# Performance work log

Measured on AMD Instinct MI355X. Metric: run time of the kernel, lower is better.

The kernel has to match this reference:

```python
import jax, jax.numpy as jnp
import numpy as np
from jax import lax

NEG_INF = -10000.0  # matches the torch code's fill value


def setup_inputs() -> dict:
    key = jax.random.key(0)
    k1, k2, k3 = jax.random.split(key, 3)
    B, T, L = 512, 512, 102  # n_labels = vocab_size(100) + 2
    logits = jax.random.normal(k1, (B, T, L), dtype=jnp.float32)
    transitions = jax.random.normal(k2, (L, L), dtype=jnp.float32)
    lens = jax.random.randint(k3, (B,), 0, 512, dtype=jnp.int32)
    return {"logits": logits, "transitions": transitions, "lens": lens}


def reference(logits, transitions, lens):
    """Linear-chain CRF partition function (forward algorithm).

    logits: [B, T, L] emission scores (L = n_labels incl. start/stop)
    transitions: [L, L], transitions[j, k] = score of k -> j
    lens: [B] int sequence lengths
    returns: [B] log partition function
    """
    B, T, L = logits.shape
    start_idx, stop_idx = L - 2, L - 1

    alpha0 = jnp.full((B, L), NEG_INF, dtype=logits.dtype).at[:, start_idx].set(0.0)

    def step(carry, logit_t):
        alpha, c_lens = carry  # alpha: [B, L], logit_t: [B, L]
        # mat[b, j, k] = transitions[j, k] + alpha[b, k]
        mat = transitions[None, :, :] + alpha[:, None, :]
        alpha_nxt = logit_t + jax.scipy.special.logsumexp(mat, axis=2)  # [B, L]
        alive = (c_lens > 0)[:, None]
        alpha = jnp.where(alive, alpha_nxt, alpha)
        return (alpha, c_lens - 1), None

    (alpha, _), _ = lax.scan(step, (alpha0, lens), jnp.swapaxes(logits, 0, 1))

    alpha = alpha + transitions[stop_idx][None, :]
    norm = jax.scipy.special.logsumexp(alpha, axis=1)  # [B]
    return norm
```

## Files before the change

kernel.cpp:

```cpp
#include <hip/hip_runtime.h>


typedef float f32x2 __attribute__((ext_vector_type(2)));
typedef float f32x4 __attribute__((ext_vector_type(4)));

#define CRF_L 102
#define CRF_RP 104
#define CRF_START 100
#define CRF_STOP 101
#define NEG_BIG (-1.0e30f)
#define LN2F 0.6931471805599453f

#define REP25(X) X(0) X(1) X(2) X(3) X(4) X(5) X(6) X(7) X(8) X(9) X(10) \
                 X(11) X(12) X(13) X(14) X(15) X(16) X(17) X(18) X(19) \
                 X(20) X(21) X(22) X(23) X(24)

template <int CTRL>
__device__ __forceinline__ float dpp_add_step(float x) {
    int xi = __builtin_bit_cast(int, x);
    int yi = __builtin_amdgcn_update_dpp(0, xi, CTRL, 0xf, 0xf, true);
    return x + __builtin_bit_cast(float, yi);
}
__device__ __forceinline__ float wave_sum64(float v) {
    v = dpp_add_step<0x111>(v);
    v = dpp_add_step<0x112>(v);
    v = dpp_add_step<0x114>(v);
    v = dpp_add_step<0x118>(v);
    v = dpp_add_step<0x142>(v);
    v = dpp_add_step<0x143>(v);
    return __builtin_bit_cast(float,
        __builtin_amdgcn_readlane(__builtin_bit_cast(int, v), 63));
}

__device__ __forceinline__ f32x2 mk2f(const float* rowp, int k, float rmx) {
    float e0 = __expf(rowp[k + 0] - rmx);
    float e1 = __expf(rowp[k + 1] - rmx);
    return (f32x2){e0, e1};
}

__attribute__((amdgpu_waves_per_eu(1, 1)))
__launch_bounds__(128)
__global__ void crf_forward_kernel(const float* __restrict__ logits,
                                   const float* __restrict__ trans,
                                   const int* __restrict__ lens,
                                   float* __restrict__ out,
                                   int B, int T) {
    const int b    = blockIdx.x;
    const int tid  = threadIdx.x;
    const int wv   = tid >> 6;
    const int lane = tid & 63;
    const bool active = (lane < 51);
    const int r    = 51 * wv + lane;

    __shared__ __align__(16) float Qbuf[2][CRF_RP];

    if (tid < 51) {
        int i0 = 2 * tid;
        Qbuf[0][i0]     = (i0 == CRF_START) ? 1.f : 0.f;
        Qbuf[0][i0 + 1] = 0.f;
    }
    if (tid == 0) { Qbuf[0][102] = 1.f; Qbuf[0][103] = 0.f; }

    const float* rowp = trans + (size_t)CRF_L * (active ? r : 0);
    float rmx = NEG_BIG;
    #pragma unroll
    for (int k = 0; k < CRF_L; ++k) rmx = fmaxf(rmx, rowp[k]);

#define DECLM(j) f32x2 m##j##a, m##j##b;
    REP25(DECLM)
#undef DECLM
    f32x2 m25a;
#define PACKJ(j) m##j##a = mk2f(rowp, 4*(j), rmx); \
                 m##j##b = mk2f(rowp, 4*(j)+2, rmx);
    REP25(PACKJ)
#undef PACKJ
    m25a = mk2f(rowp, 100, rmx);

    const float erm = active ? rmx : NEG_BIG;

    const int len = min(lens[b], T);
    const float* lgp = logits + (size_t)b * (size_t)T * (size_t)CRF_L
                              + (active ? r : 0);

    float lgA = lgp[0];
    float lgB = lgp[(size_t)min(1, T - 1) * CRF_L];
    float lgC = lgp[(size_t)min(2, T - 1) * CRF_L];

    float q    = 0.f;
    float Lacc = 0.f;

    __syncthreads();

    for (int t = 0; t < len; ++t) {
        const int cur = t & 1;
        const f32x4* P4 = reinterpret_cast<const f32x4*>(&Qbuf[cur][0]);

        f32x4 qv25 = P4[25];
        float R = qv25[2] + qv25[3];
        R = fmaxf(R, 1e-30f);
        float invRs = __builtin_amdgcn_rcpf(R) * 0.00390625f;
        float l2R = __log2f(R);

        f32x2 aL0 = {0.f,0.f}, aL1 = {0.f,0.f}, aL2 = {0.f,0.f}, aL3 = {0.f,0.f};
        f32x2 aH0 = {0.f,0.f}, aH1 = {0.f,0.f}, aH2 = {0.f,0.f}, aH3 = {0.f,0.f};
#define DOTQ(j, AL, AH) { f32x4 qv_ = P4[j]; \
        AL = __builtin_elementwise_fma(m##j##a, (f32x2){qv_[0], qv_[1]}, AL); \
        AH = __builtin_elementwise_fma(m##j##b, (f32x2){qv_[2], qv_[3]}, AH); }
        DOTQ(0,  aL0, aH0) DOTQ(1,  aL1, aH1) DOTQ(2,  aL2, aH2) DOTQ(3,  aL3, aH3)
        DOTQ(4,  aL0, aH0) DOTQ(5,  aL1, aH1) DOTQ(6,  aL2, aH2) DOTQ(7,  aL3, aH3)
        DOTQ(8,  aL0, aH0) DOTQ(9,  aL1, aH1) DOTQ(10, aL2, aH2) DOTQ(11, aL3, aH3)
        DOTQ(12, aL0, aH0) DOTQ(13, aL1, aH1) DOTQ(14, aL2, aH2) DOTQ(15, aL3, aH3)
        DOTQ(16, aL0, aH0) DOTQ(17, aL1, aH1) DOTQ(18, aL2, aH2) DOTQ(19, aL3, aH3)
        DOTQ(20, aL0, aH0) DOTQ(21, aL1, aH1) DOTQ(22, aL2, aH2) DOTQ(23, aL3, aH3)
        DOTQ(24, aL0, aH0)
#undef DOTQ
        aL1 = __builtin_elementwise_fma(m25a, (f32x2){qv25[0], qv25[1]}, aL1);

        float ec = __expf(lgA + erm);
        lgA = lgB; lgB = lgC;
        lgC = lgp[(size_t)min(t + 3, T - 1) * CRF_L];

        f32x2 tL = (aL0 + aL1) + (aL2 + aL3);
        f32x2 tH = (aH0 + aH1) + (aH2 + aH3);
        f32x2 tt = tL + tH;
        float dot = tt[0] + tt[1];

        Lacc += l2R;
        q = (dot * ec) * invRs;

        float* Qn = &Qbuf[cur ^ 1][0];
        if (active) Qn[r] = q;

        float S = wave_sum64(q);
        if (lane == 0) Qn[102 + wv] = S;

        __syncthreads();
    }

    float tsr = trans[CRF_L * CRF_STOP + (active ? r : 0)];
    float e;
    if (len == 0) {
        e = (active && r == CRF_START) ? __expf(tsr) : 0.f;
    } else {
        e = q * __expf(tsr);
    }
    float sw = wave_sum64(e);
    if (lane == 0) Qbuf[0][wv] = sw;
    __syncthreads();
    if (tid == 0)
        out[b] = LN2F * (Lacc + 8.0f * (float)len)
               + __logf(Qbuf[0][0] + Qbuf[0][1]);
}

extern "C" void kernel_launch(void* const* d_in, const int* in_sizes, int n_in,
                              void* d_out, int out_size, void* d_ws, size_t ws_size,
                              hipStream_t stream) {
    const float* logits = (const float*)d_in[0];
    const float* trans  = (const float*)d_in[1];
    const int*   lens   = (const int*)d_in[2];
    float* out = (float*)d_out;

    const int B = 512;
    const int T = 512;

    crf_forward_kernel<<<dim3(B), dim3(128), 0, stream>>>(
        logits, trans, lens, out, B, T);
}
```

Measured before the change: 377.6 us.

## Replace wave-reduced normalizer with in-loop row sum and power-of-two exponent scaling

Drops the per-step DPP wave reduction that wrote partial sums into shared memory. Each thread now sums the shared Q vector redundantly while doing the dot product. Normalisation uses an exact power-of-two scale taken from the float exponent bits, replacing rcp and log2, and the exponents are accumulated as an integer. Fewer accumulator chains are kept to save registers. The trade-off is extra adds per step and a shorter critical path per timestep.

```diff
diff --git a/kernel.cpp b/kernel.cpp
--- a/kernel.cpp
+++ b/kernel.cpp
@@ -59,7 +59,10 @@
         Qbuf[0][i0]     = (i0 == CRF_START) ? 1.f : 0.f;
         Qbuf[0][i0 + 1] = 0.f;
     }
-    if (tid == 0) { Qbuf[0][102] = 1.f; Qbuf[0][103] = 0.f; }
+    if (tid == 0) {
+        Qbuf[0][102] = 0.f; Qbuf[0][103] = 0.f;
+        Qbuf[1][102] = 0.f; Qbuf[1][103] = 0.f;
+    }
 
     const float* rowp = trans + (size_t)CRF_L * (active ? r : 0);
     float rmx = NEG_BIG;
@@ -86,8 +89,8 @@
     float lgB = lgp[(size_t)min(1, T - 1) * CRF_L];
     float lgC = lgp[(size_t)min(2, T - 1) * CRF_L];
 
-    float q    = 0.f;
-    float Lacc = 0.f;
+    float q   = 0.f;
+    int  eacc = 0;
 
     __syncthreads();
 
@@ -95,44 +98,53 @@
         const int cur = t & 1;
         const f32x4* P4 = reinterpret_cast<const f32x4*>(&Qbuf[cur][0]);
 
-        f32x4 qv25 = P4[25];
-        float R = qv25[2] + qv25[3];
-        R = fmaxf(R, 1e-30f);
-        float invRs = __builtin_amdgcn_rcpf(R) * 0.00390625f;
-        float l2R = __log2f(R);
-
-        f32x2 aL0 = {0.f,0.f}, aL1 = {0.f,0.f}, aL2 = {0.f,0.f}, aL3 = {0.f,0.f};
-        f32x2 aH0 = {0.f,0.f}, aH1 = {0.f,0.f}, aH2 = {0.f,0.f}, aH3 = {0.f,0.f};
+        f32x2 aL0 = {0.f,0.f}, aL1 = {0.f,0.f};
+        f32x2 aH0 = {0.f,0.f}, aH1 = {0.f,0.f};
+        f32x2 rs0 = {0.f,0.f}, rs1 = {0.f,0.f};
 #define DOTQ(j, AL, AH) { f32x4 qv_ = P4[j]; \
-        AL = __builtin_elementwise_fma(m##j##a, (f32x2){qv_[0], qv_[1]}, AL); \
-        AH = __builtin_elementwise_fma(m##j##b, (f32x2){qv_[2], qv_[3]}, AH); }
-        DOTQ(0,  aL0, aH0) DOTQ(1,  aL1, aH1) DOTQ(2,  aL2, aH2) DOTQ(3,  aL3, aH3)
-        DOTQ(4,  aL0, aH0) DOTQ(5,  aL1, aH1) DOTQ(6,  aL2, aH2) DOTQ(7,  aL3, aH3)
-        DOTQ(8,  aL0, aH0) DOTQ(9,  aL1, aH1) DOTQ(10, aL2, aH2) DOTQ(11, aL3, aH3)
-        DOTQ(12, aL0, aH0) DOTQ(13, aL1, aH1) DOTQ(14, aL2, aH2) DOTQ(15, aL3, aH3)
-        DOTQ(16, aL0, aH0) DOTQ(17, aL1, aH1) DOTQ(18, aL2, aH2) DOTQ(19, aL3, aH3)
-        DOTQ(20, aL0, aH0) DOTQ(21, aL1, aH1) DOTQ(22, aL2, aH2) DOTQ(23, aL3, aH3)
+        f32x2 qlo_ = (f32x2){qv_[0], qv_[1]}; \
+        f32x2 qhi_ = (f32x2){qv_[2], qv_[3]}; \
+        rs0 += qlo_; rs1 += qhi_; \
+        AL = __builtin_elementwise_fma(m##j##a, qlo_, AL); \
+        AH = __builtin_elementwise_fma(m##j##b, qhi_, AH); }
+        DOTQ(0,  aL0, aH0) DOTQ(1,  aL1, aH1)
+        DOTQ(2,  aL0, aH0) DOTQ(3,  aL1, aH1)
+        DOTQ(4,  aL0, aH0) DOTQ(5,  aL1, aH1)
+        DOTQ(6,  aL0, aH0) DOTQ(7,  aL1, aH1)
+        DOTQ(8,  aL0, aH0) DOTQ(9,  aL1, aH1)
+        DOTQ(10, aL0, aH0) DOTQ(11, aL1, aH1)
+        DOTQ(12, aL0, aH0) DOTQ(13, aL1, aH1)
+        DOTQ(14, aL0, aH0) DOTQ(15, aL1, aH1)
+        DOTQ(16, aL0, aH0) DOTQ(17, aL1, aH1)
+        DOTQ(18, aL0, aH0) DOTQ(19, aL1, aH1)
+        DOTQ(20, aL0, aH0) DOTQ(21, aL1, aH1)
+        DOTQ(22, aL0, aH0) DOTQ(23, aL1, aH1)
         DOTQ(24, aL0, aH0)
 #undef DOTQ
-        aL1 = __builtin_elementwise_fma(m25a, (f32x2){qv25[0], qv25[1]}, aL1);
+        {
+            f32x4 qv25 = P4[25];
+            f32x2 qlo_ = (f32x2){qv25[0], qv25[1]};
+            rs0 += qlo_;
+            rs1 += (f32x2){qv25[2], qv25[3]};
+            aL1 = __builtin_elementwise_fma(m25a, qlo_, aL1);
+        }
+
+        f32x2 rsv = rs0 + rs1;
+        float R = fmaxf(rsv[0] + rsv[1], 1.175494351e-38f);
+        int ef = __builtin_bit_cast(int, R) >> 23;
+        float invRs = __builtin_bit_cast(float, (246 - ef) << 23);
+        eacc += ef;
 
         float ec = __expf(lgA + erm);
+
+        f32x2 tt = (aL0 + aL1) + (aH0 + aH1);
+        float dot = tt[0] + tt[1];
+
+        q = (dot * ec) * invRs;
+        if (active) Qbuf[cur ^ 1][r] = q;
+
         lgA = lgB; lgB = lgC;
         lgC = lgp[(size_t)min(t + 3, T - 1) * CRF_L];
-
-        f32x2 tL = (aL0 + aL1) + (aL2 + aL3);
-        f32x2 tH = (aH0 + aH1) + (aH2 + aH3);
-        f32x2 tt = tL + tH;
-        float dot = tt[0] + tt[1];
-
-        Lacc += l2R;
-        q = (dot * ec) * invRs;
-
-        float* Qn = &Qbuf[cur ^ 1][0];
-        if (active) Qn[r] = q;
-
-        float S = wave_sum64(q);
-        if (lane == 0) Qn[102 + wv] = S;
 
         __syncthreads();
     }
@@ -148,7 +160,7 @@
     if (lane == 0) Qbuf[0][wv] = sw;
     __syncthreads();
     if (tid == 0)
-        out[b] = LN2F * (Lacc + 8.0f * (float)len)
+        out[b] = LN2F * ((float)eacc - 119.0f * (float)len)
                + __logf(Qbuf[0][0] + Qbuf[0][1]);
 }
 
```

New measurement: 579.0 us. 53.4% more time.

## Batch 32 sequences per block and run the CRF recurrence on fp16 MFMA

Applied to the files above, without the earlier changes.

Each block now handles 32 batch rows at once. The per-step transition product becomes a 128x32 matrix product done with seven chained 32x32x16 fp16 MFMA instructions, with the exp(transitions) operand kept in registers and the state vectors held in fp16 in shared memory. Per-row normalisation now uses power-of-two exponent scaling instead of rcp/log2, and emission logits are prefetched two steps ahead. This removes the latency-bound scalar FMA dot products, but it launches only 16 blocks, runs all T steps regardless of each sequence's length, and adds fp16 rounding to the state.

```diff
diff --git a/kernel.cpp b/kernel.cpp
--- a/kernel.cpp
+++ b/kernel.cpp
@@ -1,155 +1,150 @@
 #include <hip/hip_runtime.h>
 
 
+typedef _Float16 f16x8 __attribute__((ext_vector_type(8)));
+typedef _Float16 f16x4 __attribute__((ext_vector_type(4)));
 typedef float f32x2 __attribute__((ext_vector_type(2)));
-typedef float f32x4 __attribute__((ext_vector_type(4)));
+typedef float f32x16 __attribute__((ext_vector_type(16)));
 
 #define CRF_L 102
-#define CRF_RP 104
 #define CRF_START 100
 #define CRF_STOP 101
-#define NEG_BIG (-1.0e30f)
 #define LN2F 0.6931471805599453f
+#define QS 136
 
-#define REP25(X) X(0) X(1) X(2) X(3) X(4) X(5) X(6) X(7) X(8) X(9) X(10) \
-                 X(11) X(12) X(13) X(14) X(15) X(16) X(17) X(18) X(19) \
-                 X(20) X(21) X(22) X(23) X(24)
-
-template <int CTRL>
-__device__ __forceinline__ float dpp_add_step(float x) {
-    int xi = __builtin_bit_cast(int, x);
-    int yi = __builtin_amdgcn_update_dpp(0, xi, CTRL, 0xf, 0xf, true);
-    return x + __builtin_bit_cast(float, yi);
-}
-__device__ __forceinline__ float wave_sum64(float v) {
-    v = dpp_add_step<0x111>(v);
-    v = dpp_add_step<0x112>(v);
-    v = dpp_add_step<0x114>(v);
-    v = dpp_add_step<0x118>(v);
-    v = dpp_add_step<0x142>(v);
-    v = dpp_add_step<0x143>(v);
-    return __builtin_bit_cast(float,
-        __builtin_amdgcn_readlane(__builtin_bit_cast(int, v), 63));
-}
-
-__device__ __forceinline__ f32x2 mk2f(const float* rowp, int k, float rmx) {
-    float e0 = __expf(rowp[k + 0] - rmx);
-    float e1 = __expf(rowp[k + 1] - rmx);
-    return (f32x2){e0, e1};
-}
-
-__attribute__((amdgpu_waves_per_eu(1, 1)))
-__launch_bounds__(128)
+__launch_bounds__(256, 1)
 __global__ void crf_forward_kernel(const float* __restrict__ logits,
                                    const float* __restrict__ trans,
                                    const int* __restrict__ lens,
                                    float* __restrict__ out,
                                    int B, int T) {
-    const int b    = blockIdx.x;
+    const int b0   = blockIdx.x * 32;
     const int tid  = threadIdx.x;
     const int wv   = tid >> 6;
     const int lane = tid & 63;
-    const bool active = (lane < 51);
-    const int r    = 51 * wv + lane;
+    const int bcol = lane & 31;
+    const int h    = lane >> 5;
+    const int J    = 32 * wv + 4 * h;
 
-    __shared__ __align__(16) float Qbuf[2][CRF_RP];
+    __shared__ _Float16 Qsm[32][QS];
+    __shared__ float    Rb[2][4][64];
 
-    if (tid < 51) {
-        int i0 = 2 * tid;
-        Qbuf[0][i0]     = (i0 == CRF_START) ? 1.f : 0.f;
-        Qbuf[0][i0 + 1] = 0.f;
+    for (int i = tid; i < 32 * QS; i += 256) {
+        int c = i % QS;
+        Qsm[i / QS][c] = (_Float16)((c == CRF_START) ? 1.f : 0.f);
     }
-    if (tid == 0) { Qbuf[0][102] = 1.f; Qbuf[0][103] = 0.f; }
+    for (int i = tid; i < 2 * 4 * 64; i += 256) {
+        int buf = i >> 8, w = (i >> 6) & 3, l = i & 63;
+        Rb[buf][w][l] = (buf == 0 && w == 0 && l < 32) ? 1.f : 0.f;
+    }
 
-    const float* rowp = trans + (size_t)CRF_L * (active ? r : 0);
-    float rmx = NEG_BIG;
-    #pragma unroll
-    for (int k = 0; k < CRF_L; ++k) rmx = fmaxf(rmx, rowp[k]);
+    const int  jA   = 32 * wv + bcol;
+    const bool jAok = (jA <= 101);
+    const float* trow = trans + (size_t)CRF_L * (jAok ? jA : 0);
+    f16x8 a0, a1, a2, a3, a4, a5, a6;
+#define MKA(KT, DST) { \
+    _Pragma("unroll") \
+    for (int i = 0; i < 8; ++i) { \
+        int k = (KT)*16 + h*8 + i; \
+        float v = (jAok && k <= 101) ? __expf(trow[k]) : 0.f; \
+        DST[i] = (_Float16)v; } }
+    MKA(0, a0) MKA(1, a1) MKA(2, a2) MKA(3, a3) MKA(4, a4) MKA(5, a5) MKA(6, a6)
+#undef MKA
 
-#define DECLM(j) f32x2 m##j##a, m##j##b;
-    REP25(DECLM)
-#undef DECLM
-    f32x2 m25a;
-#define PACKJ(j) m##j##a = mk2f(rowp, 4*(j), rmx); \
-                 m##j##b = mk2f(rowp, 4*(j)+2, rmx);
-    REP25(PACKJ)
-#undef PACKJ
-    m25a = mk2f(rowp, 100, rmx);
+    const int bglob = b0 + bcol;
+    const int lenb  = min(lens[bglob], T);
+    const float* lgb = logits + (size_t)bglob * (size_t)T * CRF_L;
 
-    const float erm = active ? rmx : NEG_BIG;
+    const bool g0 = (J      <= 100), g0h = (J      <= 98);
+    const bool g1 = (J + 8  <= 100), g1h = (J + 8  <= 98);
+    const bool g2 = (J + 16 <= 100), g2h = (J + 16 <= 98);
+    const bool g3 = (J + 24 <= 100), g3h = (J + 24 <= 98);
 
-    const int len = min(lens[b], T);
-    const float* lgp = logits + (size_t)b * (size_t)T * (size_t)CRF_L
-                              + (active ? r : 0);
+#define LOADE(tt, E) { \
+    const float* p_ = lgb + (size_t)(tt) * CRF_L + J; \
+    E##0 = g0  ? *(const f32x2*)(p_ + 0)  : (f32x2){0.f, 0.f}; \
+    E##1 = g0h ? *(const f32x2*)(p_ + 2)  : (f32x2){0.f, 0.f}; \
+    E##2 = g1  ? *(const f32x2*)(p_ + 8)  : (f32x2){0.f, 0.f}; \
+    E##3 = g1h ? *(const f32x2*)(p_ + 10) : (f32x2){0.f, 0.f}; \
+    E##4 = g2  ? *(const f32x2*)(p_ + 16) : (f32x2){0.f, 0.f}; \
+    E##5 = g2h ? *(const f32x2*)(p_ + 18) : (f32x2){0.f, 0.f}; \
+    E##6 = g3  ? *(const f32x2*)(p_ + 24) : (f32x2){0.f, 0.f}; \
+    E##7 = g3h ? *(const f32x2*)(p_ + 26) : (f32x2){0.f, 0.f}; }
 
-    float lgA = lgp[0];
-    float lgB = lgp[(size_t)min(1, T - 1) * CRF_L];
-    float lgC = lgp[(size_t)min(2, T - 1) * CRF_L];
+    f32x2 eA0, eA1, eA2, eA3, eA4, eA5, eA6, eA7;
+    f32x2 eB0, eB1, eB2, eB3, eB4, eB5, eB6, eB7;
+    LOADE(0, eA)
+    LOADE(1, eB)
 
-    float q    = 0.f;
-    float Lacc = 0.f;
-
+    int iacc = 0;
     __syncthreads();
 
-    for (int t = 0; t < len; ++t) {
-        const int cur = t & 1;
-        const f32x4* P4 = reinterpret_cast<const f32x4*>(&Qbuf[cur][0]);
+#define RGRP(RG, ELO, EHI, ALIVE, SC, RS) { \
+    float e0_ = __expf(ELO[0]), e1_ = __expf(ELO[1]); \
+    float e2_ = __expf(EHI[0]), e3_ = __expf(EHI[1]); \
+    float q0_ = acc[4*(RG)+0] * e0_ * (SC); \
+    float q1_ = acc[4*(RG)+1] * e1_ * (SC); \
+    float q2_ = acc[4*(RG)+2] * e2_ * (SC); \
+    float q3_ = acc[4*(RG)+3] * e3_ * (SC); \
+    RS += (q0_ + q1_) + (q2_ + q3_); \
+    if (ALIVE) *(f16x4*)(&Qsm[bcol][J + 8*(RG)]) = \
+        (f16x4){(_Float16)q0_, (_Float16)q1_, (_Float16)q2_, (_Float16)q3_}; }
 
-        f32x4 qv25 = P4[25];
-        float R = qv25[2] + qv25[3];
-        R = fmaxf(R, 1e-30f);
-        float invRs = __builtin_amdgcn_rcpf(R) * 0.00390625f;
-        float l2R = __log2f(R);
+#define STEP(t, E) { \
+    const int cur = (t) & 1, nxt = cur ^ 1; \
+    const _Float16* qrow = &Qsm[bcol][0]; \
+    f16x8 bf0 = *(const f16x8*)(qrow + 0*16 + h*8); \
+    f16x8 bf1 = *(const f16x8*)(qrow + 1*16 + h*8); \
+    f16x8 bf2 = *(const f16x8*)(qrow + 2*16 + h*8); \
+    f16x8 bf3 = *(const f16x8*)(qrow + 3*16 + h*8); \
+    f16x8 bf4 = *(const f16x8*)(qrow + 4*16 + h*8); \
+    f16x8 bf5 = *(const f16x8*)(qrow + 5*16 + h*8); \
+    f16x8 bf6 = *(const f16x8*)(qrow + 6*16 + h*8); \
+    float R = ((Rb[cur][0][bcol] + Rb[cur][0][bcol + 32]) \
+             + (Rb[cur][1][bcol] + Rb[cur][1][bcol + 32])) \
+            + ((Rb[cur][2][bcol] + Rb[cur][2][bcol + 32]) \
+             + (Rb[cur][3][bcol] + Rb[cur][3][bcol + 32])); \
+    R = fmaxf(R, 1.175494351e-38f); \
+    int ef = __builtin_bit_cast(int, R) >> 23; \
+    float sc = __builtin_bit_cast(float, (246 - ef) << 23);   \
+    __syncthreads();    \
+    f32x16 acc = {}; \
+    acc = __builtin_amdgcn_mfma_f32_32x32x16_f16(a0, bf0, acc, 0, 0, 0); \
+    acc = __builtin_amdgcn_mfma_f32_32x32x16_f16(a1, bf1, acc, 0, 0, 0); \
+    acc = __builtin_amdgcn_mfma_f32_32x32x16_f16(a2, bf2, acc, 0, 0, 0); \
+    acc = __builtin_amdgcn_mfma_f32_32x32x16_f16(a3, bf3, acc, 0, 0, 0); \
+    acc = __builtin_amdgcn_mfma_f32_32x32x16_f16(a4, bf4, acc, 0, 0, 0); \
+    acc = __builtin_amdgcn_mfma_f32_32x32x16_f16(a5, bf5, acc, 0, 0, 0); \
+    acc = __builtin_amdgcn_mfma_f32_32x32x16_f16(a6, bf6, acc, 0, 0, 0); \
+    const bool alive = ((t) < lenb); \
+    float rsum = 0.f; \
+    RGRP(0, E##0, E##1, alive, sc, rsum) \
+    RGRP(1, E##2, E##3, alive, sc, rsum) \
+    RGRP(2, E##4, E##5, alive, sc, rsum) \
+    RGRP(3, E##6, E##7, alive, sc, rsum) \
+    Rb[nxt][wv][lane] = rsum; \
+    if (alive) iacc += ef; \
+    LOADE(min((t) + 2, T - 1), E) \
+    __syncthreads(); }
 
-        f32x2 aL0 = {0.f,0.f}, aL1 = {0.f,0.f}, aL2 = {0.f,0.f}, aL3 = {0.f,0.f};
-        f32x2 aH0 = {0.f,0.f}, aH1 = {0.f,0.f}, aH2 = {0.f,0.f}, aH3 = {0.f,0.f};
-#define DOTQ(j, AL, AH) { f32x4 qv_ = P4[j]; \
-        AL = __builtin_elementwise_fma(m##j##a, (f32x2){qv_[0], qv_[1]}, AL); \
-        AH = __builtin_elementwise_fma(m##j##b, (f32x2){qv_[2], qv_[3]}, AH); }
-        DOTQ(0,  aL0, aH0) DOTQ(1,  aL1, aH1) DOTQ(2,  aL2, aH2) DOTQ(3,  aL3, aH3)
-        DOTQ(4,  aL0, aH0) DOTQ(5,  aL1, aH1) DOTQ(6,  aL2, aH2) DOTQ(7,  aL3, aH3)
-        DOTQ(8,  aL0, aH0) DOTQ(9,  aL1, aH1) DOTQ(10, aL2, aH2) DOTQ(11, aL3, aH3)
-        DOTQ(12, aL0, aH0) DOTQ(13, aL1, aH1) DOTQ(14, aL2, aH2) DOTQ(15, aL3, aH3)
-        DOTQ(16, aL0, aH0) DOTQ(17, aL1, aH1) DOTQ(18, aL2, aH2) DOTQ(19, aL3, aH3)
-        DOTQ(20, aL0, aH0) DOTQ(21, aL1, aH1) DOTQ(22, aL2, aH2) DOTQ(23, aL3, aH3)
-        DOTQ(24, aL0, aH0)
-#undef DOTQ
-        aL1 = __builtin_elementwise_fma(m25a, (f32x2){qv25[0], qv25[1]}, aL1);
+    for (int t = 0; t < T; t += 2) {
+        STEP(t, eA)
+        STEP(t + 1, eB)
+    }
+#undef STEP
+#undef RGRP
+#undef LOADE
 
-        float ec = __expf(lgA + erm);
-        lgA = lgB; lgB = lgC;
-        lgC = lgp[(size_t)min(t + 3, T - 1) * CRF_L];
-
-        f32x2 tL = (aL0 + aL1) + (aL2 + aL3);
-        f32x2 tH = (aH0 + aH1) + (aH2 + aH3);
-        f32x2 tt = tL + tH;
-        float dot = tt[0] + tt[1];
-
-        Lacc += l2R;
-        q = (dot * ec) * invRs;
-
-        float* Qn = &Qbuf[cur ^ 1][0];
-        if (active) Qn[r] = q;
-
-        float S = wave_sum64(q);
-        if (lane == 0) Qn[102 + wv] = S;
-
-        __syncthreads();
+    if (tid < 32) {
+        const _Float16* qr = &Qsm[tid][0];
+        const float* tsp = trans + (size_t)CRF_L * CRF_STOP;
+        float dot = 0.f;
+        for (int j = 0; j < CRF_L; ++j)
+            dot += (float)qr[j] * __expf(tsp[j]);
+        int bb = b0 + tid;
+        int n = min(lens[bb], T);
+        out[bb] = __logf(dot) + LN2F * ((float)iacc - 119.0f * (float)n);
     }
-
-    float tsr = trans[CRF_L * CRF_STOP + (active ? r : 0)];
-    float e;
-    if (len == 0) {
-        e = (active && r == CRF_START) ? __expf(tsr) : 0.f;
-    } else {
-        e = q * __expf(tsr);
-    }
-    float sw = wave_sum64(e);
-    if (lane == 0) Qbuf[0][wv] = sw;
-    __syncthreads();
-    if (tid == 0)
-        out[b] = LN2F * (Lacc + 8.0f * (float)len)
-               + __logf(Qbuf[0][0] + Qbuf[0][1]);
 }
 
 extern "C" void kernel_launch(void* const* d_in, const int* in_sizes, int n_in,
@@ -163,6 +158,6 @@
     const int B = 512;
     const int T = 512;
 
-    crf_forward_kernel<<<dim3(B), dim3(128), 0, stream>>>(
+    crf_forward_kernel<<<dim3(B / 32), dim3(256), 0, stream>>>(
         logits, trans, lens, out, B, T);
 }
```

After: 723.0 us. +91.5%, slower.
